# Performance work log

Hardware: AMD Instinct MI355X
Metric: run time of the kernel (lower is better)

Reference implementation:

```python
import jax, jax.numpy as jnp
import numpy as np

ALPHA = 2.6
OPTIMAL_RANK = 1.0
SIGMA = 1.8


def setup_inputs() -> dict:
    key = jax.random.key(0)
    k1, k2 = jax.random.split(key)
    B, D, NP = 2048, 768, 8
    q_reps = jax.random.normal(k1, (B, D), dtype=jnp.float32)
    p_reps = jax.random.normal(k2, (B * NP, D), dtype=jnp.float32)
    return {"q_reps": q_reps, "p_reps": p_reps, "n_passages": NP}


def reference(q_reps, p_reps, n_passages):
    B = q_reps.shape[0]
    # [B, P] contrastive score matrix
    scores = jnp.matmul(q_reps, p_reps.T)
    target = jnp.arange(B, dtype=jnp.int32) * n_passages

    # rank position of the positive passage per query (descending argsort)
    rankings = jnp.argsort(-scores, axis=1)            # [B, P]
    positive_rankings = jnp.argmax(
        rankings == target[:, None], axis=1
    ).astype(jnp.float32)                              # [B]

    # per-sample cross-entropy (reduction='none')
    logp = jax.nn.log_softmax(scores, axis=1)
    raw_loss = -jnp.take_along_axis(logp, target[:, None], axis=1)[:, 0]

    # Gaussian rank weighting: w = 1 + alpha * exp(-(r - r_opt)^2 / (2 sigma^2))
    extra_weight = jnp.exp(-((positive_rankings - OPTIMAL_RANK) ** 2) / (2.0 * SIGMA ** 2))
    weights = 1.0 + ALPHA * extra_weight

    loss = jnp.mean(raw_loss * weights)
    return loss
```

## Files before the change

kernel.cpp:

```cpp
#include <hip/hip_runtime.h>
#include <math.h>


#define BQ 2048
#define DD 768
#define NPASS 8
#define PP 16384
#define BM 128
#define BN 256
#define BK 64
#define KITERS 12
#define NBLK 64
#define MBLK 16
#define NCHUNKS 256

#define ALPHA_C 2.6f
#define INV_2SIG2 (1.0f/6.48f)

typedef __attribute__((ext_vector_type(4))) float floatx4;

#define NQ8   196608
#define NTOT8 1769472
#define NCB   6912
__global__ __launch_bounds__(256) void prep_kernel(const float* __restrict__ qf,
                                                   const float* __restrict__ pf,
                                                   uint2* __restrict__ qb,
                                                   uint2* __restrict__ pb,
                                                   float* __restrict__ st,
                                                   float* __restrict__ out) {
  const int b = blockIdx.x;
  if (b == 0 && threadIdx.x == 0) *out = 0.f;
  if (b < NCB) {
    const int i = b * 256 + threadIdx.x;
    const float4* src; uint2* dst;
    if (i < NQ8) { src = (const float4*)qf + 2 * (size_t)i; dst = qb + i; }
    else { const size_t j = (size_t)i - NQ8; src = (const float4*)pf + 2 * j; dst = pb + j; }
    const float4 a = src[0], c = src[1];
    unsigned lo = __builtin_amdgcn_cvt_pk_fp8_f32(a.x, a.y, 0, 0);
    lo = __builtin_amdgcn_cvt_pk_fp8_f32(a.z, a.w, lo, 1);
    unsigned hi = __builtin_amdgcn_cvt_pk_fp8_f32(c.x, c.y, 0, 0);
    hi = __builtin_amdgcn_cvt_pk_fp8_f32(c.z, c.w, hi, 1);
    uint2 w; w.x = lo; w.y = hi;
    *dst = w;
  } else {
    const int wv = threadIdx.x >> 6, lane = threadIdx.x & 63;
    const int qi = (b - NCB) * 4 + wv;
    const float4* q4 = (const float4*)(qf + (size_t)qi * DD);
    const float4* p4 = (const float4*)(pf + (size_t)qi * NPASS * DD);
    float acc = 0.f;
#pragma unroll
    for (int u = 0; u < 3; ++u) {
      float4 a = q4[lane + 64 * u];
      float4 c = p4[lane + 64 * u];
      acc = fmaf(a.x, c.x, acc);
      acc = fmaf(a.y, c.y, acc);
      acc = fmaf(a.z, c.z, acc);
      acc = fmaf(a.w, c.w, acc);
    }
#pragma unroll
    for (int off = 32; off >= 1; off >>= 1) acc += __shfl_xor(acc, off);
    if (lane == 0) st[qi] = acc;
  }
}

__global__ __launch_bounds__(512) void gemm_kernel(const unsigned char* __restrict__ qb,
                                                   const unsigned char* __restrict__ pb,
                                                   const float* __restrict__ st,
                                                   float* __restrict__ pm,
                                                   float* __restrict__ pl,
                                                   float* __restrict__ pc) {
  __shared__ unsigned char As[2][8 * 1024];
  __shared__ unsigned char Bs[2][16 * 1024];
  __shared__ float st_lds[BM];

  const int t = threadIdx.x;
  const int lane = t & 63;
  const int wv = t >> 6;
  const int wm = wv >> 2, wn = wv & 3;
  const int bid = blockIdx.x;
  const int xcd = bid & 7;
  const int nb = xcd * 8 + ((bid >> 3) & 7);
  const int mb = bid >> 6;
  const int qbase = mb * BM;
  const int n0 = nb * BN;
  const int lm = lane & 15;
  const int lq = lane >> 4;
  const int lds_lane = lane * 16;

  if (t < BM) st_lds[t] = st[qbase + t];

  floatx4 acc[4][4];
#pragma unroll
  for (int i = 0; i < 4; ++i)
#pragma unroll
    for (int j = 0; j < 4; ++j) acc[i][j] = (floatx4){0.f, 0.f, 0.f, 0.f};

  const size_t arow = (size_t)(qbase + wv * 16 + lm) * DD;
  const size_t brow = (size_t)(n0 + wv * 32 + lm) * DD;

#define STAGE(KT, BUF)                                                          \
  {                                                                             \
    const size_t koff = (size_t)(KT) * BK + lq * 16;                            \
    __builtin_amdgcn_global_load_lds(                                           \
        (const __attribute__((address_space(1))) void*)(qb + arow + koff),      \
        (__attribute__((address_space(3))) void*)(&As[BUF][wv * 1024] + lds_lane), \
        16, 0, 0);                                                              \
    _Pragma("unroll")                                                           \
    for (int u = 0; u < 2; ++u) {                                               \
      __builtin_amdgcn_global_load_lds(                                         \
          (const __attribute__((address_space(1))) void*)(pb + brow + (size_t)u * 16 * DD + koff), \
          (__attribute__((address_space(3))) void*)(&Bs[BUF][(wv * 2 + u) * 1024] + lds_lane), \
          16, 0, 0);                                                            \
    }                                                                           \
  }

  STAGE(0, 0)
  for (int kt = 0; kt < KITERS; ++kt) {
    const int cb = kt & 1;
    __syncthreads();
    if (kt < KITERS - 1) STAGE(kt + 1, cb ^ 1)
#pragma unroll
    for (int ks = 0; ks < 2; ++ks) {
      const int intra = (ks * 2 + (lq >> 1)) * 256 + lm * 16 + (lq & 1) * 8;
      long a[4], b[4];
#pragma unroll
      for (int i = 0; i < 4; ++i)
        a[i] = *(const long*)(&As[cb][(wm * 4 + i) * 1024] + intra);
#pragma unroll
      for (int j = 0; j < 4; ++j)
        b[j] = *(const long*)(&Bs[cb][(wn * 4 + j) * 1024] + intra);
#pragma unroll
      for (int i = 0; i < 4; ++i)
#pragma unroll
        for (int j = 0; j < 4; ++j)
          acc[i][j] = __builtin_amdgcn_mfma_f32_16x16x32_fp8_fp8(a[i], b[j], acc[i][j], 0, 0, 0);
    }
  }

  const int chunk = nb * 4 + wn;
  float* const pmc = pm + (size_t)chunk * BQ;
  float* const plc = pl + (size_t)chunk * BQ;
  float* const pcc = pc + (size_t)chunk * BQ;
#pragma unroll
  for (int i = 0; i < 4; ++i) {
#pragma unroll
    for (int r = 0; r < 4; ++r) {
      const int rl = wm * 64 + i * 16 + lq * 4 + r;
      float mx = fmaxf(fmaxf(acc[i][0][r], acc[i][1][r]),
                       fmaxf(acc[i][2][r], acc[i][3][r]));
#pragma unroll
      for (int off = 1; off <= 8; off <<= 1) mx = fmaxf(mx, __shfl_xor(mx, off));
      const float stv = st_lds[rl];
      const int qg = qbase + rl;
      const int tcol = qg * NPASS;
      float sum = 0.f, c = 0.f;
#pragma unroll
      for (int j = 0; j < 4; ++j) {
        const float s = acc[i][j][r];
        sum += __expf(s - mx);
        const int cg = n0 + wn * 64 + j * 16 + lm;
        if (s > stv && cg != tcol) c += 1.f;
      }
#pragma unroll
      for (int off = 1; off <= 8; off <<= 1) {
        sum += __shfl_xor(sum, off);
        c += __shfl_xor(c, off);
      }
      if (lm == 0) {
        pmc[qg] = mx; plc[qg] = sum; pcc[qg] = c;
      }
    }
  }
}

__global__ __launch_bounds__(256) void finalize_kernel(const float* __restrict__ st,
                                                       const float* __restrict__ pm,
                                                       const float* __restrict__ pl,
                                                       const float* __restrict__ pc,
                                                       float* __restrict__ out) {
  const int wv = threadIdx.x >> 6, lane = threadIdx.x & 63;
  const int q = blockIdx.x * 64 + lane;
  const int c0 = wv * 64;
  float m = -1e30f, l = 0.f, c = 0.f;
#pragma unroll 4
  for (int ch = 0; ch < 64; ++ch) {
    const size_t idx = (size_t)(c0 + ch) * BQ + q;
    const float mv = pm[idx], lv = pl[idx], cv = pc[idx];
    const float nm = fmaxf(m, mv);
    l = l * __expf(m - nm) + lv * __expf(mv - nm);
    m = nm; c += cv;
  }
  __shared__ float sm[4][64], sl[4][64], sc[4][64];
  sm[wv][lane] = m; sl[wv][lane] = l; sc[wv][lane] = c;
  __syncthreads();
  if (wv == 0) {
    float M = sm[0][lane], L = sl[0][lane], C = sc[0][lane];
#pragma unroll
    for (int w = 1; w < 4; ++w) {
      const float mv = sm[w][lane];
      const float nm = fmaxf(M, mv);
      L = L * __expf(M - nm) + sl[w][lane] * __expf(mv - nm);
      M = nm; C += sc[w][lane];
    }
    const float raw = logf(L) + M - st[q];
    const float dr = C - 1.0f;
    const float w = 1.0f + ALPHA_C * __expf(-(dr * dr) * INV_2SIG2);
    float loss = raw * w * (1.0f / (float)BQ);
#pragma unroll
    for (int off = 32; off >= 1; off >>= 1) loss += __shfl_xor(loss, off);
    if (lane == 0) atomicAdd(out, loss);
  }
}

extern "C" void kernel_launch(void* const* d_in, const int* in_sizes, int n_in,
                              void* d_out, int out_size, void* d_ws, size_t ws_size,
                              hipStream_t stream) {
  const float* q = (const float*)d_in[0];
  const float* p = (const float*)d_in[1];
  char* ws = (char*)d_ws;
  unsigned char* qb = (unsigned char*)ws;
  unsigned char* pb = (unsigned char*)(ws + 1572864);
  float* st = (float*)(ws + 14155776);
  float* pm = (float*)(ws + 14163968);
  float* pl = (float*)(ws + 16261120);
  float* pc = (float*)(ws + 18358272);
  float* out = (float*)d_out;

  prep_kernel<<<NCB + BQ / 4, 256, 0, stream>>>(q, p, (uint2*)qb, (uint2*)pb, st, out);
  gemm_kernel<<<NBLK * MBLK, 512, 0, stream>>>(qb, pb, st, pm, pl, pc);
  finalize_kernel<<<BQ / 64, 256, 0, stream>>>(st, pm, pl, pc, out);
}
```

Before: 180.9 us.

## Enlarge GEMM block tile to 256 rows and add triple-buffered LDS pipeline

The fp8 GEMM block now covers 256 query rows instead of 128, using 16 waves (1024 threads), so each B tile staged in LDS is reused across twice as many rows. The double-buffered K loop becomes a three-stage ring buffer that prefetches two K-steps ahead. It uses explicit vmcnt waits, raw s_barrier and sched_barrier to overlap global-to-LDS loads with MFMA work. The cost is 96KB of LDS and half as many blocks (512), which can hurt occupancy and load balance across CUs. The hand-placed waitcnt also relies on the exact number of loads issued per stage.

```diff
diff --git a/kernel.cpp b/kernel.cpp
--- a/kernel.cpp
+++ b/kernel.cpp
@@ -6,12 +6,12 @@
 #define DD 768
 #define NPASS 8
 #define PP 16384
-#define BM 128
+#define BM 256
 #define BN 256
 #define BK 64
 #define KITERS 12
 #define NBLK 64
-#define MBLK 16
+#define MBLK 8
 #define NCHUNKS 256
 
 #define ALPHA_C 2.6f
@@ -63,14 +63,14 @@
   }
 }
 
-__global__ __launch_bounds__(512) void gemm_kernel(const unsigned char* __restrict__ qb,
-                                                   const unsigned char* __restrict__ pb,
-                                                   const float* __restrict__ st,
-                                                   float* __restrict__ pm,
-                                                   float* __restrict__ pl,
-                                                   float* __restrict__ pc) {
-  __shared__ unsigned char As[2][8 * 1024];
-  __shared__ unsigned char Bs[2][16 * 1024];
+__global__ __launch_bounds__(1024) void gemm_kernel(const unsigned char* __restrict__ qb,
+                                                    const unsigned char* __restrict__ pb,
+                                                    const float* __restrict__ st,
+                                                    float* __restrict__ pm,
+                                                    float* __restrict__ pl,
+                                                    float* __restrict__ pc) {
+  __shared__ unsigned char As[3][16 * 1024];
+  __shared__ unsigned char Bs[3][16 * 1024];
   __shared__ float st_lds[BM];
 
   const int t = threadIdx.x;
@@ -96,7 +96,7 @@
     for (int j = 0; j < 4; ++j) acc[i][j] = (floatx4){0.f, 0.f, 0.f, 0.f};
 
   const size_t arow = (size_t)(qbase + wv * 16 + lm) * DD;
-  const size_t brow = (size_t)(n0 + wv * 32 + lm) * DD;
+  const size_t brow = (size_t)(n0 + wv * 16 + lm) * DD;
 
 #define STAGE(KT, BUF)                                                          \
   {                                                                             \
@@ -105,37 +105,47 @@
         (const __attribute__((address_space(1))) void*)(qb + arow + koff),      \
         (__attribute__((address_space(3))) void*)(&As[BUF][wv * 1024] + lds_lane), \
         16, 0, 0);                                                              \
+    __builtin_amdgcn_global_load_lds(                                           \
+        (const __attribute__((address_space(1))) void*)(pb + brow + koff),      \
+        (__attribute__((address_space(3))) void*)(&Bs[BUF][wv * 1024] + lds_lane), \
+        16, 0, 0);                                                              \
+  }
+
+#define COMPUTE(CB)                                                             \
+  _Pragma("unroll")                                                             \
+  for (int ks = 0; ks < 2; ++ks) {                                              \
+    const int intra = (ks * 2 + (lq >> 1)) * 256 + lm * 16 + (lq & 1) * 8;      \
+    long a[4], b[4];                                                            \
     _Pragma("unroll")                                                           \
-    for (int u = 0; u < 2; ++u) {                                               \
-      __builtin_amdgcn_global_load_lds(                                         \
-          (const __attribute__((address_space(1))) void*)(pb + brow + (size_t)u * 16 * DD + koff), \
-          (__attribute__((address_space(3))) void*)(&Bs[BUF][(wv * 2 + u) * 1024] + lds_lane), \
-          16, 0, 0);                                                            \
-    }                                                                           \
+    for (int i = 0; i < 4; ++i)                                                 \
+      a[i] = *(const long*)(&As[CB][(wm * 4 + i) * 1024] + intra);              \
+    _Pragma("unroll")                                                           \
+    for (int j = 0; j < 4; ++j)                                                 \
+      b[j] = *(const long*)(&Bs[CB][(wn * 4 + j) * 1024] + intra);              \
+    _Pragma("unroll")                                                           \
+    for (int i = 0; i < 4; ++i)                                                 \
+      _Pragma("unroll")                                                         \
+      for (int j = 0; j < 4; ++j)                                               \
+        acc[i][j] = __builtin_amdgcn_mfma_f32_16x16x32_fp8_fp8(a[i], b[j], acc[i][j], 0, 0, 0); \
   }
 
   STAGE(0, 0)
-  for (int kt = 0; kt < KITERS; ++kt) {
-    const int cb = kt & 1;
-    __syncthreads();
-    if (kt < KITERS - 1) STAGE(kt + 1, cb ^ 1)
-#pragma unroll
-    for (int ks = 0; ks < 2; ++ks) {
-      const int intra = (ks * 2 + (lq >> 1)) * 256 + lm * 16 + (lq & 1) * 8;
-      long a[4], b[4];
-#pragma unroll
-      for (int i = 0; i < 4; ++i)
-        a[i] = *(const long*)(&As[cb][(wm * 4 + i) * 1024] + intra);
-#pragma unroll
-      for (int j = 0; j < 4; ++j)
-        b[j] = *(const long*)(&Bs[cb][(wn * 4 + j) * 1024] + intra);
-#pragma unroll
-      for (int i = 0; i < 4; ++i)
-#pragma unroll
-        for (int j = 0; j < 4; ++j)
-          acc[i][j] = __builtin_amdgcn_mfma_f32_16x16x32_fp8_fp8(a[i], b[j], acc[i][j], 0, 0, 0);
-    }
-  }
+  STAGE(1, 1)
+  int cur = 0;
+  int stg = 2;
+  for (int kt = 0; kt < KITERS - 1; ++kt) {
+    asm volatile("s_waitcnt vmcnt(2)" ::: "memory");
+    __builtin_amdgcn_s_barrier();
+    __builtin_amdgcn_sched_barrier(0);
+    if (kt < KITERS - 2) STAGE(kt + 2, stg)
+    COMPUTE(cur)
+    cur = (cur == 2) ? 0 : cur + 1;
+    stg = (stg == 2) ? 0 : stg + 1;
+  }
+  asm volatile("s_waitcnt vmcnt(0)" ::: "memory");
+  __builtin_amdgcn_s_barrier();
+  __builtin_amdgcn_sched_barrier(0);
+  COMPUTE(cur)
 
   const int chunk = nb * 4 + wn;
   float* const pmc = pm + (size_t)chunk * BQ;
@@ -227,6 +237,6 @@
   float* out = (float*)d_out;
 
   prep_kernel<<<NCB + BQ / 4, 256, 0, stream>>>(q, p, (uint2*)qb, (uint2*)pb, st, out);
-  gemm_kernel<<<NBLK * MBLK, 512, 0, stream>>>(qb, pb, st, pm, pl, pc);
+  gemm_kernel<<<NBLK * MBLK, 1024, 0, stream>>>(qb, pb, st, pm, pl, pc);
   finalize_kernel<<<BQ / 64, 256, 0, stream>>>(st, pm, pl, pc, out);
 }
```

Result: faster. 152.9 us (-15.5%).

## Switch FP8 GEMM to 32x32x64 scaled MFMA with 256x256 tiles

Applied to the files above, without the earlier changes.

Replaces the 16x16x32 FP8 MFMA with the gfx950 scaled 32x32x64 f8f6f4 MFMA, enlarges the block tile to 256x256 with BK=128 and 1024 threads, and unifies A/B staging into one LDS buffer where each wave loads 32 rows. The aim is to cut LDS fragment reads and instruction count per FLOP and to halve the grid's redundant loads. It also adds manual waitcnt/barrier scheduling and setprio. The risks are lower occupancy from 128KB of LDS per block and a grid of only 512 blocks on 256 CUs.

```diff
diff --git a/kernel.cpp b/kernel.cpp
--- a/kernel.cpp
+++ b/kernel.cpp
@@ -6,18 +6,20 @@
 #define DD 768
 #define NPASS 8
 #define PP 16384
-#define BM 128
+#define BM 256
 #define BN 256
-#define BK 64
-#define KITERS 12
+#define BK 128
+#define KITERS 6
 #define NBLK 64
-#define MBLK 16
+#define MBLK 8
 #define NCHUNKS 256
 
 #define ALPHA_C 2.6f
 #define INV_2SIG2 (1.0f/6.48f)
 
-typedef __attribute__((ext_vector_type(4))) float floatx4;
+typedef __attribute__((ext_vector_type(16))) float floatx16;
+typedef __attribute__((ext_vector_type(4))) int intx4;
+typedef __attribute__((ext_vector_type(8))) int intx8;
 
 #define NQ8   196608
 #define NTOT8 1769472
@@ -63,14 +65,13 @@
   }
 }
 
-__global__ __launch_bounds__(512) void gemm_kernel(const unsigned char* __restrict__ qb,
-                                                   const unsigned char* __restrict__ pb,
-                                                   const float* __restrict__ st,
-                                                   float* __restrict__ pm,
-                                                   float* __restrict__ pl,
-                                                   float* __restrict__ pc) {
-  __shared__ unsigned char As[2][8 * 1024];
-  __shared__ unsigned char Bs[2][16 * 1024];
+__global__ __launch_bounds__(1024) void gemm_kernel(const unsigned char* __restrict__ qb,
+                                                    const unsigned char* __restrict__ pb,
+                                                    const float* __restrict__ st,
+                                                    float* __restrict__ pm,
+                                                    float* __restrict__ pl,
+                                                    float* __restrict__ pc) {
+  __shared__ unsigned char Ts[2][16 * 4096];
   __shared__ float st_lds[BM];
 
   const int t = threadIdx.x;
@@ -83,90 +84,96 @@
   const int mb = bid >> 6;
   const int qbase = mb * BM;
   const int n0 = nb * BN;
-  const int lm = lane & 15;
-  const int lq = lane >> 4;
-  const int lds_lane = lane * 16;
+  const int lm32 = lane & 31;
+  const int lhi = lane >> 5;
 
   if (t < BM) st_lds[t] = st[qbase + t];
 
-  floatx4 acc[4][4];
-#pragma unroll
-  for (int i = 0; i < 4; ++i)
-#pragma unroll
-    for (int j = 0; j < 4; ++j) acc[i][j] = (floatx4){0.f, 0.f, 0.f, 0.f};
-
-  const size_t arow = (size_t)(qbase + wv * 16 + lm) * DD;
-  const size_t brow = (size_t)(n0 + wv * 32 + lm) * DD;
+  floatx16 acc[2][2];
+#pragma unroll
+  for (int i = 0; i < 2; ++i)
+#pragma unroll
+    for (int j = 0; j < 2; ++j)
+#pragma unroll
+      for (int r = 0; r < 16; ++r) acc[i][j][r] = 0.f;
+
+  const int srow = (wv < 8) ? (qbase + wv * 32) : (n0 + (wv - 8) * 32);
+  const unsigned char* const sbase =
+      ((wv < 8) ? qb : pb) + (size_t)(srow + lm32) * DD;
 
 #define STAGE(KT, BUF)                                                          \
   {                                                                             \
-    const size_t koff = (size_t)(KT) * BK + lq * 16;                            \
-    __builtin_amdgcn_global_load_lds(                                           \
-        (const __attribute__((address_space(1))) void*)(qb + arow + koff),      \
-        (__attribute__((address_space(3))) void*)(&As[BUF][wv * 1024] + lds_lane), \
-        16, 0, 0);                                                              \
     _Pragma("unroll")                                                           \
-    for (int u = 0; u < 2; ++u) {                                               \
+    for (int v = 0; v < 4; ++v) {                                               \
       __builtin_amdgcn_global_load_lds(                                         \
-          (const __attribute__((address_space(1))) void*)(pb + brow + (size_t)u * 16 * DD + koff), \
-          (__attribute__((address_space(3))) void*)(&Bs[BUF][(wv * 2 + u) * 1024] + lds_lane), \
+          (const __attribute__((address_space(1))) void*)(sbase + (KT) * BK + (2 * v + lhi) * 16), \
+          (__attribute__((address_space(3))) void*)(&Ts[BUF][wv * 4096 + v * 1024] + lane * 16), \
           16, 0, 0);                                                            \
     }                                                                           \
+  }
+
+#define FRAG(dst, CBUF, UNIT, H)                                                \
+  {                                                                             \
+    const unsigned char* ub = &Ts[CBUF][(UNIT) * 4096] +                        \
+                              ((H) * 4 + lhi * 2) * 512 + lm32 * 16;            \
+    intx4 lo = *(const intx4*)ub;                                               \
+    intx4 hi = *(const intx4*)(ub + 512);                                       \
+    dst = __builtin_shufflevector(lo, hi, 0, 1, 2, 3, 4, 5, 6, 7);              \
+  }
+
+#define COMPUTE(CBUF)                                                           \
+  _Pragma("unroll")                                                             \
+  for (int h = 0; h < 2; ++h) {                                                 \
+    intx8 af[2], bf[2];                                                         \
+    FRAG(af[0], CBUF, wm * 2 + 0, h)                                            \
+    FRAG(af[1], CBUF, wm * 2 + 1, h)                                            \
+    FRAG(bf[0], CBUF, 8 + wn * 2 + 0, h)                                        \
+    FRAG(bf[1], CBUF, 8 + wn * 2 + 1, h)                                        \
+    __builtin_amdgcn_s_setprio(1);                                              \
+    acc[0][0] = __builtin_amdgcn_mfma_scale_f32_32x32x64_f8f6f4(af[0], bf[0], acc[0][0], 0, 0, 0, 127, 0, 127); \
+    acc[0][1] = __builtin_amdgcn_mfma_scale_f32_32x32x64_f8f6f4(af[0], bf[1], acc[0][1], 0, 0, 0, 127, 0, 127); \
+    acc[1][0] = __builtin_amdgcn_mfma_scale_f32_32x32x64_f8f6f4(af[1], bf[0], acc[1][0], 0, 0, 0, 127, 0, 127); \
+    acc[1][1] = __builtin_amdgcn_mfma_scale_f32_32x32x64_f8f6f4(af[1], bf[1], acc[1][1], 0, 0, 0, 127, 0, 127); \
+    __builtin_amdgcn_s_setprio(0);                                              \
   }
 
   STAGE(0, 0)
   for (int kt = 0; kt < KITERS; ++kt) {
     const int cb = kt & 1;
-    __syncthreads();
+    asm volatile("s_waitcnt vmcnt(0)" ::: "memory");
+    __builtin_amdgcn_s_barrier();
+    __builtin_amdgcn_sched_barrier(0);
     if (kt < KITERS - 1) STAGE(kt + 1, cb ^ 1)
-#pragma unroll
-    for (int ks = 0; ks < 2; ++ks) {
-      const int intra = (ks * 2 + (lq >> 1)) * 256 + lm * 16 + (lq & 1) * 8;
-      long a[4], b[4];
-#pragma unroll
-      for (int i = 0; i < 4; ++i)
-        a[i] = *(const long*)(&As[cb][(wm * 4 + i) * 1024] + intra);
-#pragma unroll
-      for (int j = 0; j < 4; ++j)
-        b[j] = *(const long*)(&Bs[cb][(wn * 4 + j) * 1024] + intra);
-#pragma unroll
-      for (int i = 0; i < 4; ++i)
-#pragma unroll
-        for (int j = 0; j < 4; ++j)
-          acc[i][j] = __builtin_amdgcn_mfma_f32_16x16x32_fp8_fp8(a[i], b[j], acc[i][j], 0, 0, 0);
-    }
+    if (cb == 0) { COMPUTE(0) } else { COMPUTE(1) }
   }
 
   const int chunk = nb * 4 + wn;
   float* const pmc = pm + (size_t)chunk * BQ;
   float* const plc = pl + (size_t)chunk * BQ;
   float* const pcc = pc + (size_t)chunk * BQ;
-#pragma unroll
-  for (int i = 0; i < 4; ++i) {
-#pragma unroll
-    for (int r = 0; r < 4; ++r) {
-      const int rl = wm * 64 + i * 16 + lq * 4 + r;
-      float mx = fmaxf(fmaxf(acc[i][0][r], acc[i][1][r]),
-                       fmaxf(acc[i][2][r], acc[i][3][r]));
-#pragma unroll
-      for (int off = 1; off <= 8; off <<= 1) mx = fmaxf(mx, __shfl_xor(mx, off));
+  const int cgbase = n0 + wn * 64 + lm32;
+#pragma unroll
+  for (int i = 0; i < 2; ++i) {
+#pragma unroll
+    for (int r = 0; r < 16; ++r) {
+      const int rl = wm * 64 + i * 32 + (r & 3) + 8 * (r >> 2) + 4 * lhi;
+      const float s0 = acc[i][0][r], s1 = acc[i][1][r];
+      float mx = fmaxf(s0, s1);
+#pragma unroll
+      for (int off = 1; off <= 16; off <<= 1) mx = fmaxf(mx, __shfl_xor(mx, off));
       const float stv = st_lds[rl];
       const int qg = qbase + rl;
       const int tcol = qg * NPASS;
-      float sum = 0.f, c = 0.f;
-#pragma unroll
-      for (int j = 0; j < 4; ++j) {
-        const float s = acc[i][j][r];
-        sum += __expf(s - mx);
-        const int cg = n0 + wn * 64 + j * 16 + lm;
-        if (s > stv && cg != tcol) c += 1.f;
-      }
-#pragma unroll
-      for (int off = 1; off <= 8; off <<= 1) {
+      float sum = __expf(s0 - mx) + __expf(s1 - mx);
+      float c = 0.f;
+      if (s0 > stv && cgbase != tcol) c += 1.f;
+      if (s1 > stv && cgbase + 32 != tcol) c += 1.f;
+#pragma unroll
+      for (int off = 1; off <= 16; off <<= 1) {
         sum += __shfl_xor(sum, off);
         c += __shfl_xor(c, off);
       }
-      if (lm == 0) {
+      if (lm32 == 0) {
         pmc[qg] = mx; plc[qg] = sum; pcc[qg] = c;
       }
     }
@@ -227,6 +234,6 @@
   float* out = (float*)d_out;
 
   prep_kernel<<<NCB + BQ / 4, 256, 0, stream>>>(q, p, (uint2*)qb, (uint2*)pb, st, out);
-  gemm_kernel<<<NBLK * MBLK, 512, 0, stream>>>(qb, pb, st, pm, pl, pc);
+  gemm_kernel<<<NBLK * MBLK, 1024, 0, stream>>>(qb, pb, st, pm, pl, pc);
   finalize_kernel<<<BQ / 64, 256, 0, stream>>>(st, pm, pl, pc, out);
 }
```

Measured after the change: 364.6 us. 102% more time.
